# Performance work log

Measured on AMD Instinct MI355X. Metric: run time of the kernel, lower is better.

## Reference

```python
import jax, jax.numpy as jnp
import numpy as np

GAMMA = 0.01
INFER_STEP = 4
C, B, G, S, L = 8, 32, 2048, 32, 3


def softor(x, axis, gamma=GAMMA):
    # gamma-weighted soft-or: gamma * logsumexp(x/gamma); renormalize if max > 1
    lse = gamma * jax.nn.logsumexp(x / gamma, axis=axis)
    m = jnp.max(lse)
    return jnp.where(m > 1.0, lse / m, lse)


def clause_fn(I_i, x):
    # I_i: [G, S, L] int indices into atom axis; x: [B, G]
    gathered = jnp.take(x, I_i, axis=1)        # [B, G, S, L]
    body = jnp.prod(gathered, axis=3)          # [B, G, S] (AND over body literals)
    return softor(body, axis=2)                # [B, G]   (OR over substitutions)


def setup_inputs() -> dict:
    key = jax.random.key(0)
    k1, k2 = jax.random.split(key)
    x = jax.random.uniform(k1, (B, G), dtype=jnp.float32)
    I = jax.random.randint(k2, (C, G, S, L), 0, G)
    return {"x": x, "I": I}


def reference(x, I):
    # R: [C, B, G] per-clause valuations, initialized from x
    R = jnp.broadcast_to(x[None], (C, B, G))
    r = jax.vmap(clause_fn)  # map over clause axis of I and R
    for _ in range(INFER_STEP):
        R = softor(jnp.stack([R, r(I, R)], axis=1), axis=1)
    return R
```

## Files before the change

### kernel.cpp

```cpp
#include <hip/hip_runtime.h>
#include <hip/hip_bf16.h>
#include <hip/hip_fp16.h>

#define C_ 8
#define B_ 32
#define G_ 2048
#define S_ 32
#define L_ 3
#define GB_ (G_ * B_)


#define OFF_BUF0 0
#define OFF_BUF1 524288
#define OFF_MAX  1048576
#define OFF_GMAX (OFF_MAX + 512)
#define ZERO_FLOATS 576

#define K_SCALE 144.26950408889634f
#define GLN2 0.0069314718055994531f

#define EXP2F(x) __builtin_amdgcn_exp2f(x)
#define LOG2F(x) __builtin_amdgcn_logf(x)

__device__ __forceinline__ void atomicMaxPos(float* a, float v) {
    atomicMax((unsigned*)a, __float_as_uint(v));
}

__device__ __forceinline__ uint2 pack4h(float4 v) {
    __half2 a = __floats2half2_rn(v.x, v.y);
    __half2 b = __floats2half2_rn(v.z, v.w);
    uint2 q;
    q.x = *reinterpret_cast<unsigned*>(&a);
    q.y = *reinterpret_cast<unsigned*>(&b);
    return q;
}
__device__ __forceinline__ float4 unpack4h(uint2 q) {
    __half2 a = *reinterpret_cast<__half2*>(&q.x);
    __half2 b = *reinterpret_cast<__half2*>(&q.y);
    float2 fa = __half22float2(a), fb = __half22float2(b);
    return make_float4(fa.x, fa.y, fb.x, fb.y);
}

__device__ __forceinline__ float4 body3(float4 a, float4 b, float4 c) {
    float4 r;
    r.x = a.x * b.x * (c.x * K_SCALE);
    r.y = a.y * b.y * (c.y * K_SCALE);
    r.z = a.z * b.z * (c.z * K_SCALE);
    r.w = a.w * b.w * (c.w * K_SCALE);
    return r;
}
__device__ __forceinline__ float4 fmax4v(float4 a, float4 b) {
    float4 r;
    r.x = fmaxf(a.x, b.x); r.y = fmaxf(a.y, b.y);
    r.z = fmaxf(a.z, b.z); r.w = fmaxf(a.w, b.w);
    return r;
}
__device__ __forceinline__ float4 exp2m(float4 a, float4 m) {
    float4 r;
    r.x = EXP2F(a.x - m.x); r.y = EXP2F(a.y - m.y);
    r.z = EXP2F(a.z - m.z); r.w = EXP2F(a.w - m.w);
    return r;
}

__global__ __launch_bounds__(256, 2) void k_clause(const float* __restrict__ Rbase,
                                                   int xmode,
                                                   const int* __restrict__ I,
                                                   float* __restrict__ r_out,
                                                   const float* __restrict__ gmax_prev,
                                                   float* __restrict__ cmax_step) {
    __shared__ unsigned sRh[G_ * 2];
    __shared__ float sRed[4];

    const int tid = threadIdx.x;
    const int bid = blockIdx.x;
    const int c = bid >> 6;
    const int bh = (bid >> 3) & 7;
    const int gs = bid & 7;

    const float gm = gmax_prev ? gmax_prev[0] : 0.0f;
    const float sc = (gm > 1.0f) ? (1.0f / gm) : 1.0f;

    if (xmode) {
        const int j = tid >> 6;
        const int g0 = tid & 63;
        const float* xr = Rbase + (bh * 4 + j) * G_;
        __half* sH = (__half*)sRh;
#pragma unroll
        for (int k = 0; k < 32; ++k) {
            const int g = g0 + 64 * k;
            sH[g * 4 + j] = __float2half_rn(xr[g]);
        }
    } else {
        const float4* src = (const float4*)(Rbase + c * GB_ + bh * (G_ * 4));
        uint2* dst = (uint2*)sRh;
#pragma unroll
        for (int k = 0; k < 8; ++k) {
            float4 v = src[tid + k * 256];
            v.x *= sc; v.y *= sc; v.z *= sc; v.w *= sc;
            dst[tid + k * 256] = pack4h(v);
        }
    }
    __syncthreads();

    const uint2* sH2 = (const uint2*)sRh;
    const int row = gs * 256 + tid;
    const int4* p = (const int4*)(I + (c * G_ + row) * 96);

    float4 lm[8], pp[8];
#pragma unroll
    for (int ch = 0; ch < 8; ++ch) {
        const int4 qa = p[ch * 3 + 0], qb = p[ch * 3 + 1], qc = p[ch * 3 + 2];
        const float4 b0 = body3(unpack4h(sH2[qa.x]), unpack4h(sH2[qa.y]), unpack4h(sH2[qa.z]));
        const float4 b1 = body3(unpack4h(sH2[qa.w]), unpack4h(sH2[qb.x]), unpack4h(sH2[qb.y]));
        const float4 b2 = body3(unpack4h(sH2[qb.z]), unpack4h(sH2[qb.w]), unpack4h(sH2[qc.x]));
        const float4 b3 = body3(unpack4h(sH2[qc.y]), unpack4h(sH2[qc.z]), unpack4h(sH2[qc.w]));
        const float4 l = fmax4v(fmax4v(b0, b1), fmax4v(b2, b3));
        const float4 e0 = exp2m(b0, l), e1 = exp2m(b1, l);
        const float4 e2 = exp2m(b2, l), e3 = exp2m(b3, l);
        float4 s;
        s.x = e0.x + e1.x + e2.x + e3.x;
        s.y = e0.y + e1.y + e2.y + e3.y;
        s.z = e0.z + e1.z + e2.z + e3.z;
        s.w = e0.w + e1.w + e2.w + e3.w;
        lm[ch] = l; pp[ch] = s;
    }
    float4 M = fmax4v(fmax4v(fmax4v(lm[0], lm[1]), fmax4v(lm[2], lm[3])),
                      fmax4v(fmax4v(lm[4], lm[5]), fmax4v(lm[6], lm[7])));
    float4 sum = make_float4(0.f, 0.f, 0.f, 0.f);
#pragma unroll
    for (int ch = 0; ch < 8; ++ch) {
        const float4 w = exp2m(lm[ch], M);
        sum.x += pp[ch].x * w.x; sum.y += pp[ch].y * w.y;
        sum.z += pp[ch].z * w.z; sum.w += pp[ch].w * w.w;
    }
    float4 lse;
    lse.x = GLN2 * (M.x + LOG2F(sum.x));
    lse.y = GLN2 * (M.y + LOG2F(sum.y));
    lse.z = GLN2 * (M.z + LOG2F(sum.z));
    lse.w = GLN2 * (M.w + LOG2F(sum.w));

    *(float4*)(r_out + ((c * 8 + bh) * G_ + row) * 4) = lse;

    float m = fmaxf(fmaxf(lse.x, lse.y), fmaxf(lse.z, lse.w));
#pragma unroll
    for (int o = 32; o; o >>= 1) m = fmaxf(m, __shfl_xor(m, o, 64));
    const int lane = tid & 63, wv = tid >> 6;
    if (lane == 0) sRed[wv] = m;
    __syncthreads();
    if (tid == 0) {
        float a = fmaxf(fmaxf(sRed[0], sRed[1]), fmaxf(sRed[2], sRed[3]));
        atomicMaxPos(&cmax_step[c * 16], a);
    }
}

__global__ __launch_bounds__(256, 8) void k_combine(const float* __restrict__ Rold,
                                                    int xmode,
                                                    const float* __restrict__ r_in,
                                                    float* __restrict__ Rnew,
                                                    const float* __restrict__ gmax_prev,
                                                    const float* __restrict__ cmax_step,
                                                    float* __restrict__ gmax_out) {
    __shared__ float sRed[4];
    const int tid = threadIdx.x;
    const int i4 = (blockIdx.x * 256 + tid) * 4;
    const int c = i4 >> 16;

    const float gm = gmax_prev ? gmax_prev[0] : 0.0f;
    const float sc = (gm > 1.0f) ? (1.0f / gm) : 1.0f;
    const float cmv = cmax_step[c * 16];
    const float scr = (cmv > 1.0f) ? (1.0f / cmv) : 1.0f;

    float4 Ro;
    if (xmode) {
        const int w = i4 & (GB_ - 1);
        const int bq = w >> 13;
        const int g = (w & 8191) >> 2;
        Ro.x = Rold[(bq * 4 + 0) * G_ + g];
        Ro.y = Rold[(bq * 4 + 1) * G_ + g];
        Ro.z = Rold[(bq * 4 + 2) * G_ + g];
        Ro.w = Rold[(bq * 4 + 3) * G_ + g];
    } else {
        Ro = *(const float4*)(Rold + i4);
    }
    const float4 rv = *(const float4*)(r_in + i4);
    float4 o;
    {
        float Rn = Ro.x * sc, rn = rv.x * scr;
        float M = fmaxf(Rn, rn), mn = fminf(Rn, rn);
        o.x = M + 0.01f * __logf(1.0f + __expf((mn - M) * 100.0f));
    }
    {
        float Rn = Ro.y * sc, rn = rv.y * scr;
        float M = fmaxf(Rn, rn), mn = fminf(Rn, rn);
        o.y = M + 0.01f * __logf(1.0f + __expf((mn - M) * 100.0f));
    }
    {
        float Rn = Ro.z * sc, rn = rv.z * scr;
        float M = fmaxf(Rn, rn), mn = fminf(Rn, rn);
        o.z = M + 0.01f * __logf(1.0f + __expf((mn - M) * 100.0f));
    }
    {
        float Rn = Ro.w * sc, rn = rv.w * scr;
        float M = fmaxf(Rn, rn), mn = fminf(Rn, rn);
        o.w = M + 0.01f * __logf(1.0f + __expf((mn - M) * 100.0f));
    }
    *(float4*)(Rnew + i4) = o;

    float mm = fmaxf(fmaxf(o.x, o.y), fmaxf(o.z, o.w));
#pragma unroll
    for (int off = 32; off; off >>= 1) mm = fmaxf(mm, __shfl_xor(mm, off, 64));
    const int lane = tid & 63, wv = tid >> 6;
    if (lane == 0) sRed[wv] = mm;
    __syncthreads();
    if (tid == 0) {
        float a = fmaxf(fmaxf(sRed[0], sRed[1]), fmaxf(sRed[2], sRed[3]));
        atomicMaxPos(gmax_out, a);
    }
}

__global__ __launch_bounds__(256) void k_out(const float* __restrict__ buf0,
                                             const float* __restrict__ gmaxslot,
                                             float* __restrict__ out) {
    __shared__ float sT[32 * 65];
    const int bid = blockIdx.x;
    const int c = bid >> 5;
    const int g0 = (bid & 31) << 6;
    const int tid = threadIdx.x;

    const float gm = gmaxslot[0];
    const float sc = (gm > 1.0f) ? (1.0f / gm) : 1.0f;

    const int r = tid >> 2, w = tid & 3;
#pragma unroll
    for (int k = 0; k < 8; ++k) {
        sT[(k * 4 + w) * 65 + r] = buf0[((c * 8 + k) * G_ + g0 + r) * 4 + w] * sc;
    }
    __syncthreads();
#pragma unroll
    for (int k = 0; k < 8; ++k) {
        const int j = tid + k * 256;
        const int b = j >> 6, gg = j & 63;
        out[(c * B_ + b) * G_ + g0 + gg] = sT[b * 65 + gg];
    }
}

extern "C" void kernel_launch(void* const* d_in, const int* in_sizes, int n_in,
                              void* d_out, int out_size, void* d_ws, size_t ws_size,
                              hipStream_t stream) {
    const float* x = (const float*)d_in[0];
    const int* I = (const int*)d_in[1];
    float* out = (float*)d_out;
    float* ws = (float*)d_ws;

    float* buf0 = ws + OFF_BUF0;
    float* buf1 = ws + OFF_BUF1;
    float* maxs = ws + OFF_MAX;
    float* gmax = ws + OFF_GMAX;

    hipMemsetAsync(ws + OFF_MAX, 0, ZERO_FLOATS * sizeof(float), stream);

    for (int t = 0; t < 4; ++t) {
        const float* Rsrc = (t == 0) ? x : buf0;
        const int xmode = (t == 0) ? 1 : 0;
        const float* gprev = (t == 0) ? nullptr : (gmax + (t - 1) * 16);
        float* cstep = maxs + t * 128;

        k_clause<<<512, 256, 0, stream>>>(Rsrc, xmode, I, buf1, gprev, cstep);
        k_combine<<<512, 256, 0, stream>>>(Rsrc, xmode, buf1, buf0, gprev, cstep,
                                           gmax + t * 16);
    }

    k_out<<<256, 256, 0, stream>>>(buf0, gmax + 48, out);
}
```

Baseline: 93.80 us.

## Split each row's substitution chunks across 8 lanes with shuffle logsumexp reduction

The clause kernel now assigns each of a row's 8 substitution chunks to a separate lane, with 8 rows per wave per pass, instead of having one thread walk all 32 substitutions of a row. Neighbouring lanes then read contiguous index data, which coalesces the global loads of I, and each thread holds far fewer live registers. The max and sum of the logsumexp are combined across the 8 lanes with xor shuffles. In exchange it adds shuffle traffic, an 8-pass loop that is not unrolled, and stores from only one lane in eight.

```diff
diff --git a/kernel.cpp b/kernel.cpp
--- a/kernel.cpp
+++ b/kernel.cpp
@@ -59,6 +59,12 @@
     float4 r;
     r.x = EXP2F(a.x - m.x); r.y = EXP2F(a.y - m.y);
     r.z = EXP2F(a.z - m.z); r.w = EXP2F(a.w - m.w);
+    return r;
+}
+__device__ __forceinline__ float4 shflx4(float4 v, int m) {
+    float4 r;
+    r.x = __shfl_xor(v.x, m, 64); r.y = __shfl_xor(v.y, m, 64);
+    r.z = __shfl_xor(v.z, m, 64); r.w = __shfl_xor(v.w, m, 64);
     return r;
 }
 
@@ -103,48 +109,64 @@
     __syncthreads();
 
     const uint2* sH2 = (const uint2*)sRh;
-    const int row = gs * 256 + tid;
-    const int4* p = (const int4*)(I + (c * G_ + row) * 96);
-
-    float4 lm[8], pp[8];
-#pragma unroll
-    for (int ch = 0; ch < 8; ++ch) {
-        const int4 qa = p[ch * 3 + 0], qb = p[ch * 3 + 1], qc = p[ch * 3 + 2];
+    const int wv = tid >> 6;
+    const int lane = tid & 63;
+    const int ch = lane & 7;
+    const int rl = lane >> 3;
+
+    float blockm = -1e30f;
+
+#pragma unroll 1
+    for (int pass = 0; pass < 8; ++pass) {
+        const int row = gs * 256 + wv * 64 + pass * 8 + rl;
+        const int4* P = (const int4*)(I + (c * G_ + row) * 96);
+        const int4 qa = P[ch * 3 + 0], qb = P[ch * 3 + 1], qc = P[ch * 3 + 2];
+
         const float4 b0 = body3(unpack4h(sH2[qa.x]), unpack4h(sH2[qa.y]), unpack4h(sH2[qa.z]));
         const float4 b1 = body3(unpack4h(sH2[qa.w]), unpack4h(sH2[qb.x]), unpack4h(sH2[qb.y]));
         const float4 b2 = body3(unpack4h(sH2[qb.z]), unpack4h(sH2[qb.w]), unpack4h(sH2[qc.x]));
         const float4 b3 = body3(unpack4h(sH2[qc.y]), unpack4h(sH2[qc.z]), unpack4h(sH2[qc.w]));
-        const float4 l = fmax4v(fmax4v(b0, b1), fmax4v(b2, b3));
-        const float4 e0 = exp2m(b0, l), e1 = exp2m(b1, l);
-        const float4 e2 = exp2m(b2, l), e3 = exp2m(b3, l);
+
+        const float4 lm = fmax4v(fmax4v(b0, b1), fmax4v(b2, b3));
+        const float4 e0 = exp2m(b0, lm), e1 = exp2m(b1, lm);
+        const float4 e2 = exp2m(b2, lm), e3 = exp2m(b3, lm);
+        float4 pp;
+        pp.x = e0.x + e1.x + e2.x + e3.x;
+        pp.y = e0.y + e1.y + e2.y + e3.y;
+        pp.z = e0.z + e1.z + e2.z + e3.z;
+        pp.w = e0.w + e1.w + e2.w + e3.w;
+
+        float4 M = lm;
+        M = fmax4v(M, shflx4(M, 1));
+        M = fmax4v(M, shflx4(M, 2));
+        M = fmax4v(M, shflx4(M, 4));
+        const float4 w4 = exp2m(lm, M);
         float4 s;
-        s.x = e0.x + e1.x + e2.x + e3.x;
-        s.y = e0.y + e1.y + e2.y + e3.y;
-        s.z = e0.z + e1.z + e2.z + e3.z;
-        s.w = e0.w + e1.w + e2.w + e3.w;
-        lm[ch] = l; pp[ch] = s;
-    }
-    float4 M = fmax4v(fmax4v(fmax4v(lm[0], lm[1]), fmax4v(lm[2], lm[3])),
-                      fmax4v(fmax4v(lm[4], lm[5]), fmax4v(lm[6], lm[7])));
-    float4 sum = make_float4(0.f, 0.f, 0.f, 0.f);
-#pragma unroll
-    for (int ch = 0; ch < 8; ++ch) {
-        const float4 w = exp2m(lm[ch], M);
-        sum.x += pp[ch].x * w.x; sum.y += pp[ch].y * w.y;
-        sum.z += pp[ch].z * w.z; sum.w += pp[ch].w * w.w;
-    }
-    float4 lse;
-    lse.x = GLN2 * (M.x + LOG2F(sum.x));
-    lse.y = GLN2 * (M.y + LOG2F(sum.y));
-    lse.z = GLN2 * (M.z + LOG2F(sum.z));
-    lse.w = GLN2 * (M.w + LOG2F(sum.w));
-
-    *(float4*)(r_out + ((c * 8 + bh) * G_ + row) * 4) = lse;
-
-    float m = fmaxf(fmaxf(lse.x, lse.y), fmaxf(lse.z, lse.w));
+        s.x = pp.x * w4.x; s.y = pp.y * w4.y;
+        s.z = pp.z * w4.z; s.w = pp.w * w4.w;
+        {
+            float4 t1 = shflx4(s, 1);
+            s.x += t1.x; s.y += t1.y; s.z += t1.z; s.w += t1.w;
+            float4 t2 = shflx4(s, 2);
+            s.x += t2.x; s.y += t2.y; s.z += t2.z; s.w += t2.w;
+            float4 t4 = shflx4(s, 4);
+            s.x += t4.x; s.y += t4.y; s.z += t4.z; s.w += t4.w;
+        }
+        float4 lse;
+        lse.x = GLN2 * (M.x + LOG2F(s.x));
+        lse.y = GLN2 * (M.y + LOG2F(s.y));
+        lse.z = GLN2 * (M.z + LOG2F(s.z));
+        lse.w = GLN2 * (M.w + LOG2F(s.w));
+
+        if (ch == 0)
+            *(float4*)(r_out + ((c * 8 + bh) * G_ + row) * 4) = lse;
+
+        blockm = fmaxf(blockm, fmaxf(fmaxf(lse.x, lse.y), fmaxf(lse.z, lse.w)));
+    }
+
+    float m = blockm;
 #pragma unroll
     for (int o = 32; o; o >>= 1) m = fmaxf(m, __shfl_xor(m, o, 64));
-    const int lane = tid & 63, wv = tid >> 6;
     if (lane == 0) sRed[wv] = m;
     __syncthreads();
     if (tid == 0) {
```

Result: slower. 105.3 us (+12.3%).
